# Performance work log

Hardware: AMD Instinct MI355X
Metric: run time of the kernel (lower is better)

Reference implementation:

```python
import jax, jax.numpy as jnp
import numpy as np

EMBED_DIM = 1024
NUM_HEADS = 16
HEAD_DIM = EMBED_DIM // NUM_HEADS


def setup_inputs() -> dict:
    key = jax.random.key(0)
    ks = jax.random.split(key, 7)
    B, S, E = 2, 2048, EMBED_DIM
    # xavier_uniform bound for square [E, E] weight
    bound = float(np.sqrt(6.0 / (E + E)))
    mkw = lambda k: jax.random.uniform(k, (E, E), jnp.float32, -bound, bound)
    return {
        "query": jax.random.normal(ks[0], (B, S, E), jnp.float32),
        "key": jax.random.normal(ks[1], (B, S, E), jnp.float32),
        "value": jax.random.normal(ks[2], (B, S, E), jnp.float32),
        "Wq": mkw(ks[3]),
        "Wk": mkw(ks[4]),
        "Wv": mkw(ks[5]),
        "Wo": mkw(ks[6]),
    }


def reference(query, key, value, Wq, Wk, Wv, Wo):
    # Chunked sigmoid attention: since sigmoid has no cross-key normalization
    # and all projections are bias-free linear maps, summing per-KV-chunk
    # partial outputs is mathematically identical to the full computation:
    #   out = (sigmoid(scale * Q K^T) @ V) @ Wo^T
    B, L, E = query.shape
    H, D = NUM_HEADS, HEAD_DIM
    scale = D ** -0.5
    q = (query @ Wq.T).reshape(B, L, H, D) * scale   # [B,L,H,D]
    k = (key @ Wk.T).reshape(B, -1, H, D)            # [B,S,H,D]
    v = (value @ Wv.T).reshape(B, -1, H, D)          # [B,S,H,D]
    scores = jax.nn.sigmoid(jnp.einsum('blhd,bshd->bhls', q, k))  # [B,H,L,S]
    o = jnp.einsum('bhls,bshd->blhd', scores, v).reshape(B, L, E)
    return o @ Wo.T
```

## Files before the change

### kernel.cpp

```cpp
#include <hip/hip_runtime.h>

typedef float f32x4 __attribute__((ext_vector_type(4)));
typedef float f32x16 __attribute__((ext_vector_type(16)));
typedef __bf16 bf16x4 __attribute__((ext_vector_type(4)));
typedef __bf16 bf16x8 __attribute__((ext_vector_type(8)));

constexpr int E = 1024;
constexpr int S = 2048;
constexpr int Bsz = 2;
constexpr int H = 16;
constexpr int Dh = 64;
constexpr int M = Bsz * S;

#define GLOAD_LDS16(g, l)                                                                 \
  __builtin_amdgcn_global_load_lds((const __attribute__((address_space(1))) void*)(g),    \
                                   (__attribute__((address_space(3))) void*)(l), 16, 0, 0)

__device__ __forceinline__ unsigned pk2(float a, float b) {
  union { __bf16 h[2]; unsigned u; } r;
  r.h[0] = (__bf16)a; r.h[1] = (__bf16)b;
  return r.u;
}

__global__ __launch_bounds__(256) void convert_bf16(
    const float* __restrict__ q, const float* __restrict__ k,
    const float* __restrict__ v, const float* __restrict__ wq,
    const float* __restrict__ wk, const float* __restrict__ wv,
    const float* __restrict__ wo, __bf16* __restrict__ aq,
    __bf16* __restrict__ ak, __bf16* __restrict__ av,
    __bf16* __restrict__ wqkv, __bf16* __restrict__ wob) {
  const int id = blockIdx.y;
  const float* src;
  __bf16* dst;
  int n;
  float scale = 1.0f;
  switch (id) {
    case 0: src = q;  dst = aq;             n = M * E; break;
    case 1: src = k;  dst = ak;             n = M * E; break;
    case 2: src = v;  dst = av;             n = M * E; break;
    case 3: src = wq; dst = wqkv;           n = E * E; scale = 0.125f; break;
    case 4: src = wk; dst = wqkv + E * E;   n = E * E; break;
    case 5: src = wv; dst = wqkv + 2 * E * E; n = E * E; break;
    default: src = wo; dst = wob;           n = E * E; break;
  }
  const int stride = gridDim.x * 256 * 8;
  for (int i = (blockIdx.x * 256 + threadIdx.x) * 8; i < n; i += stride) {
    f32x4 a = *reinterpret_cast<const f32x4*>(&src[i]);
    f32x4 b = *reinterpret_cast<const f32x4*>(&src[i + 4]);
    bf16x8 o;
    o[0] = (__bf16)(a[0] * scale); o[1] = (__bf16)(a[1] * scale);
    o[2] = (__bf16)(a[2] * scale); o[3] = (__bf16)(a[3] * scale);
    o[4] = (__bf16)(b[0] * scale); o[5] = (__bf16)(b[1] * scale);
    o[6] = (__bf16)(b[2] * scale); o[7] = (__bf16)(b[3] * scale);
    *reinterpret_cast<bf16x8*>(&dst[i]) = o;
  }
}

template <int TM, int MODE>
__global__ __launch_bounds__(256) void gemm_bf16nt(
    const __bf16* __restrict__ A0, const __bf16* __restrict__ A1,
    const __bf16* __restrict__ A2, const __bf16* __restrict__ Bw,
    void* __restrict__ C0, void* __restrict__ C1, void* __restrict__ C2) {
  constexpr int MI = TM / 32;
  __shared__ __bf16 As[TM][64];
  __shared__ __bf16 Bs[128][64];

  const int t    = threadIdx.x;
  const int lane = t & 63;
  const int wid  = t >> 6;
  const int wr   = (wid >> 1) * (TM / 2);
  const int wc   = (wid & 1) * 64;
  const int r16  = lane & 15;
  const int tm   = blockIdx.y * TM;
  const int tn   = blockIdx.x * 128;
  const int which = tn >> 10;

  const __bf16* Ab = (MODE == 0) ? (which == 0 ? A0 : which == 1 ? A1 : A2) : A0;

  f32x4 acc[MI][4] = {};

  for (int kt = 0; kt < E / 64; ++kt) {
    const int k0 = kt * 64;
    __syncthreads();
    constexpr int ACH = TM / 8;
    constexpr int NCH = ACH + 16;
#pragma unroll
    for (int c = wid; c < NCH; c += 4) {
      const bool isA = c < ACH;
      const int cc   = isA ? c : c - ACH;
      const int L    = cc * 1024 + lane * 16;
      const int row  = L >> 7;
      const int sw   = ((L >> 4) & 7) ^ (row & 7);
      const __bf16* src = isA ? &Ab[(size_t)(tm + row) * E + k0 + sw * 8]
                              : &Bw[(size_t)(tn + row) * E + k0 + sw * 8];
      char* dst = (isA ? (char*)As : (char*)Bs) + cc * 1024;
      GLOAD_LDS16(src, dst);
    }
    __syncthreads();
#pragma unroll
    for (int kc = 0; kc < 2; ++kc) {
      bf16x8 af[MI], bfv[4];
#pragma unroll
      for (int mi = 0; mi < MI; ++mi) {
        int row = wr + mi * 16 + r16;
        int g   = (kc * 4 + (lane >> 4)) ^ (row & 7);
        af[mi] = *reinterpret_cast<const bf16x8*>(&As[row][g * 8]);
      }
#pragma unroll
      for (int ni = 0; ni < 4; ++ni) {
        int row = wc + ni * 16 + r16;
        int g   = (kc * 4 + (lane >> 4)) ^ (row & 7);
        bfv[ni] = *reinterpret_cast<const bf16x8*>(&Bs[row][g * 8]);
      }
#pragma unroll
      for (int mi = 0; mi < MI; ++mi)
#pragma unroll
        for (int ni = 0; ni < 4; ++ni)
          acc[mi][ni] = __builtin_amdgcn_mfma_f32_16x16x32_bf16(af[mi], bfv[ni],
                                                                acc[mi][ni], 0, 0, 0);
    }
  }

#pragma unroll
  for (int mi = 0; mi < MI; ++mi) {
#pragma unroll
    for (int ni = 0; ni < 4; ++ni) {
#pragma unroll
      for (int j = 0; j < 4; ++j) {
        float v = acc[mi][ni][j];
        int m = tm + wr + mi * 16 + ((lane >> 4) << 2) + j;
        int n = tn + wc + ni * 16 + r16;
        if constexpr (MODE == 0) {
          int nl = n & 1023;
          int b = m >> 11, s = m & 2047, h = nl >> 6, d = nl & 63;
          __bf16* Cout = which == 0 ? (__bf16*)C0 : which == 1 ? (__bf16*)C1
                                                              : (__bf16*)C2;
          if (which < 2)
            Cout[((size_t)(b * H + h) * S + s) * Dh + d] = (__bf16)v;
          else
            Cout[((size_t)(b * H + h) * Dh + d) * S + s] = (__bf16)v;
        } else {
          ((float*)C0)[(size_t)m * E + n] = v;
        }
      }
    }
  }
}

__global__ __launch_bounds__(256) void attn_sigmoid(const __bf16* __restrict__ Q,
                                                    const __bf16* __restrict__ K,
                                                    const __bf16* __restrict__ Vt,
                                                    __bf16* __restrict__ O) {
  __shared__ char smem[128 * 72 * 2];
  __bf16* Ks = (__bf16*)smem;
  __bf16* Vs = (__bf16*)(smem + 8192);
  __bf16* Os = (__bf16*)smem;

  const int t    = threadIdx.x;
  const int lane = t & 63;
  const int wid  = t >> 6;
  const int l31  = lane & 31;
  const int hh   = lane >> 5;
  const int q0   = blockIdx.x * 128;
  const int h    = blockIdx.y;
  const int b    = blockIdx.z;

  const __bf16* Qh = Q + (size_t)(b * H + h) * S * Dh;
  const __bf16* Kh = K + (size_t)(b * H + h) * S * Dh;
  const __bf16* Vh = Vt + (size_t)(b * H + h) * Dh * S;

  bf16x8 Qf[4];
#pragma unroll
  for (int kc = 0; kc < 4; ++kc)
    Qf[kc] = *reinterpret_cast<const bf16x8*>(
        &Qh[(size_t)(q0 + wid * 32 + l31) * Dh + kc * 16 + hh * 8]);

  f32x16 ot[2] = {};

  for (int st = 0; st < S / 64; ++st) {
    __syncthreads();
#pragma unroll
    for (int j = 0; j < 2; ++j) {
      int base = (wid * 2 + j) * 1024;
      int L    = base + lane * 16;
      int row  = L >> 7;
      int x    = (L >> 4) & 7;
      int sw   = ((x ^ (row & 7)) * 8);
      GLOAD_LDS16(&Kh[(size_t)(st * 64 + row) * Dh + sw], (char*)Ks + base);
      GLOAD_LDS16(&Vh[(size_t)row * S + st * 64 + sw], (char*)Vs + base);
    }
    __syncthreads();

#pragma unroll
    for (int si = 0; si < 2; ++si) {
      f32x16 sacc = {};
#pragma unroll
      for (int kc = 0; kc < 4; ++kc) {
        int row = si * 32 + l31;
        int x = (2 * kc + hh) ^ (row & 7);
        bf16x8 kf = *reinterpret_cast<const bf16x8*>(&Ks[row * 64 + x * 8]);
        sacc = __builtin_amdgcn_mfma_f32_32x32x16_bf16(kf, Qf[kc], sacc, 0, 0, 0);
      }
      float p[16];
#pragma unroll
      for (int r = 0; r < 16; ++r)
        p[r] = __builtin_amdgcn_rcpf(1.0f + __expf(-sacc[r]));
      unsigned A0 = pk2(p[0], p[1]),   A1 = pk2(p[2], p[3]);
      unsigned B0 = pk2(p[4], p[5]),   B1 = pk2(p[6], p[7]);
      unsigned C0 = pk2(p[8], p[9]),   C1 = pk2(p[10], p[11]);
      unsigned D0 = pk2(p[12], p[13]), D1 = pk2(p[14], p[15]);
      unsigned W0 = __shfl_xor((int)(hh ? A0 : B0), 32, 64);
      unsigned W1 = __shfl_xor((int)(hh ? A1 : B1), 32, 64);
      unsigned W2 = __shfl_xor((int)(hh ? C0 : D0), 32, 64);
      unsigned W3 = __shfl_xor((int)(hh ? C1 : D1), 32, 64);
      union { unsigned u[4]; bf16x8 v; } f0, f1;
      f0.u[0] = hh ? W0 : A0;  f0.u[1] = hh ? W1 : A1;
      f0.u[2] = hh ? B0 : W0;  f0.u[3] = hh ? B1 : W1;
      f1.u[0] = hh ? W2 : C0;  f1.u[1] = hh ? W3 : C1;
      f1.u[2] = hh ? D0 : W2;  f1.u[3] = hh ? D1 : W3;

#pragma unroll
      for (int dblk = 0; dblk < 2; ++dblk) {
        int row = dblk * 32 + l31;
        int c0 = si * 2;
        int x0 = (2 * c0 + hh) ^ (row & 7);
        int x1 = (2 * (c0 + 1) + hh) ^ (row & 7);
        bf16x8 vf0 = *reinterpret_cast<const bf16x8*>(&Vs[row * 64 + x0 * 8]);
        bf16x8 vf1 = *reinterpret_cast<const bf16x8*>(&Vs[row * 64 + x1 * 8]);
        ot[dblk] = __builtin_amdgcn_mfma_f32_32x32x16_bf16(vf0, f0.v, ot[dblk], 0, 0, 0);
        ot[dblk] = __builtin_amdgcn_mfma_f32_32x32x16_bf16(vf1, f1.v, ot[dblk], 0, 0, 0);
      }
    }
  }

  __syncthreads();
#pragma unroll
  for (int dblk = 0; dblk < 2; ++dblk) {
#pragma unroll
    for (int rp = 0; rp < 8; ++rp) {
      int r = rp * 2;
      int d0 = dblk * 32 + (r & 3) + 8 * (r >> 2) + 4 * hh;
      unsigned u = pk2(ot[dblk][r], ot[dblk][r + 1]);
      *reinterpret_cast<unsigned*>(&Os[(wid * 32 + l31) * 72 + d0]) = u;
    }
  }
  __syncthreads();
#pragma unroll
  for (int i = 0; i < 4; ++i) {
    int c = i * 256 + t;
    int row = c >> 3;
    int ch = c & 7;
    bf16x8 v = *reinterpret_cast<const bf16x8*>(&Os[row * 72 + ch * 8]);
    *reinterpret_cast<bf16x8*>(&O[((size_t)(b * S) + q0 + row) * E + h * Dh + ch * 8]) = v;
  }
}

extern "C" void kernel_launch(void* const* d_in, const int* in_sizes, int n_in,
                              void* d_out, int out_size, void* d_ws, size_t ws_size,
                              hipStream_t stream) {
  const float* query = (const float*)d_in[0];
  const float* key_  = (const float*)d_in[1];
  const float* value = (const float*)d_in[2];
  const float* Wq    = (const float*)d_in[3];
  const float* Wk    = (const float*)d_in[4];
  const float* Wv    = (const float*)d_in[5];
  const float* Wo    = (const float*)d_in[6];

  char* ws = (char*)d_ws;
  __bf16* aq   = (__bf16*)(ws);
  __bf16* ak   = (__bf16*)(ws + ((size_t)8 << 20));
  __bf16* av   = (__bf16*)(ws + ((size_t)16 << 20));
  __bf16* wqkv = (__bf16*)(ws + ((size_t)24 << 20));
  __bf16* wob  = (__bf16*)(ws + ((size_t)30 << 20));
  __bf16* pq   = (__bf16*)(ws + ((size_t)32 << 20));
  __bf16* pk   = (__bf16*)(ws + ((size_t)40 << 20));
  __bf16* pvt  = (__bf16*)(ws + ((size_t)48 << 20));
  __bf16* ob   = (__bf16*)(ws);

  convert_bf16<<<dim3(512, 7), 256, 0, stream>>>(query, key_, value, Wq, Wk, Wv,
                                                 Wo, aq, ak, av, wqkv, wob);

  gemm_bf16nt<128, 0><<<dim3(3072 / 128, M / 128), 256, 0, stream>>>(
      aq, ak, av, wqkv, pq, pk, pvt);

  attn_sigmoid<<<dim3(S / 128, H, Bsz), 256, 0, stream>>>(pq, pk, pvt, ob);

  gemm_bf16nt<64, 2><<<dim3(E / 128, M / 64), 256, 0, stream>>>(
      ob, nullptr, nullptr, wob, (float*)d_out, nullptr, nullptr);
}
```

Before: 160.1 us.

## Double-buffer K/V tiles in sigmoid attention and fold log2e into Q scale

The attention kernel now uses 128-thread blocks over 64 query rows and double-buffers K/V tiles in LDS, issuing the next tile's async loads before computing the current one. This leaves one barrier per iteration. The Q weight scale now includes -log2(e), so sigmoid becomes rcp(1+exp2(x)) with no negate or multiply. The V-transpose store permutes sequence indices so the P fragments feed the PV MFMA directly without cross-lane shuffles. Output staging uses an XOR-swizzled LDS layout, and setprio hints are placed around the MFMA phases. The trade-off is more blocks, each holding 32KB of LDS, and a tighter coupling between the projection GEMM's store layout and the attention kernel.

```diff
diff --git a/kernel.cpp b/kernel.cpp
--- a/kernel.cpp
+++ b/kernel.cpp
@@ -38,7 +38,7 @@
     case 0: src = q;  dst = aq;             n = M * E; break;
     case 1: src = k;  dst = ak;             n = M * E; break;
     case 2: src = v;  dst = av;             n = M * E; break;
-    case 3: src = wq; dst = wqkv;           n = E * E; scale = 0.125f; break;
+    case 3: src = wq; dst = wqkv;           n = E * E; scale = -0.18033688f; break;
     case 4: src = wk; dst = wqkv + E * E;   n = E * E; break;
     case 5: src = wv; dst = wqkv + 2 * E * E; n = E * E; break;
     default: src = wo; dst = wob;           n = E * E; break;
@@ -135,10 +135,12 @@
           int b = m >> 11, s = m & 2047, h = nl >> 6, d = nl & 63;
           __bf16* Cout = which == 0 ? (__bf16*)C0 : which == 1 ? (__bf16*)C1
                                                               : (__bf16*)C2;
-          if (which < 2)
+          if (which < 2) {
             Cout[((size_t)(b * H + h) * S + s) * Dh + d] = (__bf16)v;
-          else
-            Cout[((size_t)(b * H + h) * Dh + d) * S + s] = (__bf16)v;
+          } else {
+            int ssw = (s & ~12) | ((s & 4) << 1) | ((s & 8) >> 1);
+            Cout[((size_t)(b * H + h) * Dh + d) * S + ssw] = (__bf16)v;
+          }
         } else {
           ((float*)C0)[(size_t)m * E + n] = v;
         }
@@ -147,21 +149,18 @@
   }
 }
 
-__global__ __launch_bounds__(256) void attn_sigmoid(const __bf16* __restrict__ Q,
+__global__ __launch_bounds__(128) void attn_sigmoid(const __bf16* __restrict__ Q,
                                                     const __bf16* __restrict__ K,
                                                     const __bf16* __restrict__ Vt,
                                                     __bf16* __restrict__ O) {
-  __shared__ char smem[128 * 72 * 2];
-  __bf16* Ks = (__bf16*)smem;
-  __bf16* Vs = (__bf16*)(smem + 8192);
-  __bf16* Os = (__bf16*)smem;
+  __shared__ char smem[2][16384];
 
   const int t    = threadIdx.x;
   const int lane = t & 63;
   const int wid  = t >> 6;
   const int l31  = lane & 31;
   const int hh   = lane >> 5;
-  const int q0   = blockIdx.x * 128;
+  const int q0   = blockIdx.x * 64;
   const int h    = blockIdx.y;
   const int b    = blockIdx.z;
 
@@ -169,88 +168,118 @@
   const __bf16* Kh = K + (size_t)(b * H + h) * S * Dh;
   const __bf16* Vh = Vt + (size_t)(b * H + h) * Dh * S;
 
+  auto stage = [&](int st, int pb) {
+    char* bK = &smem[pb][0];
+    char* bV = &smem[pb][8192];
+#pragma unroll
+    for (int j = 0; j < 4; ++j) {
+      int base = (wid * 4 + j) * 1024;
+      int L    = base + lane * 16;
+      int row  = L >> 7;
+      int sw   = ((L >> 4) & 7) ^ (row & 7);
+      GLOAD_LDS16(&Kh[(size_t)(st * 64 + row) * Dh + sw * 8], bK + base);
+      GLOAD_LDS16(&Vh[(size_t)row * S + st * 64 + sw * 8], bV + base);
+    }
+  };
+
+  stage(0, 0);
+
   bf16x8 Qf[4];
 #pragma unroll
   for (int kc = 0; kc < 4; ++kc)
     Qf[kc] = *reinterpret_cast<const bf16x8*>(
         &Qh[(size_t)(q0 + wid * 32 + l31) * Dh + kc * 16 + hh * 8]);
 
-  f32x16 ot[2] = {};
+  f32x16 ot0 = {}, ot1 = {};
+  __syncthreads();
 
   for (int st = 0; st < S / 64; ++st) {
-    __syncthreads();
-#pragma unroll
-    for (int j = 0; j < 2; ++j) {
-      int base = (wid * 2 + j) * 1024;
-      int L    = base + lane * 16;
-      int row  = L >> 7;
-      int x    = (L >> 4) & 7;
-      int sw   = ((x ^ (row & 7)) * 8);
-      GLOAD_LDS16(&Kh[(size_t)(st * 64 + row) * Dh + sw], (char*)Ks + base);
-      GLOAD_LDS16(&Vh[(size_t)row * S + st * 64 + sw], (char*)Vs + base);
-    }
-    __syncthreads();
-
-#pragma unroll
-    for (int si = 0; si < 2; ++si) {
-      f32x16 sacc = {};
-#pragma unroll
-      for (int kc = 0; kc < 4; ++kc) {
-        int row = si * 32 + l31;
-        int x = (2 * kc + hh) ^ (row & 7);
-        bf16x8 kf = *reinterpret_cast<const bf16x8*>(&Ks[row * 64 + x * 8]);
-        sacc = __builtin_amdgcn_mfma_f32_32x32x16_bf16(kf, Qf[kc], sacc, 0, 0, 0);
-      }
-      float p[16];
-#pragma unroll
-      for (int r = 0; r < 16; ++r)
-        p[r] = __builtin_amdgcn_rcpf(1.0f + __expf(-sacc[r]));
-      unsigned A0 = pk2(p[0], p[1]),   A1 = pk2(p[2], p[3]);
-      unsigned B0 = pk2(p[4], p[5]),   B1 = pk2(p[6], p[7]);
-      unsigned C0 = pk2(p[8], p[9]),   C1 = pk2(p[10], p[11]);
-      unsigned D0 = pk2(p[12], p[13]), D1 = pk2(p[14], p[15]);
-      unsigned W0 = __shfl_xor((int)(hh ? A0 : B0), 32, 64);
-      unsigned W1 = __shfl_xor((int)(hh ? A1 : B1), 32, 64);
-      unsigned W2 = __shfl_xor((int)(hh ? C0 : D0), 32, 64);
-      unsigned W3 = __shfl_xor((int)(hh ? C1 : D1), 32, 64);
-      union { unsigned u[4]; bf16x8 v; } f0, f1;
-      f0.u[0] = hh ? W0 : A0;  f0.u[1] = hh ? W1 : A1;
-      f0.u[2] = hh ? B0 : W0;  f0.u[3] = hh ? B1 : W1;
-      f1.u[0] = hh ? W2 : C0;  f1.u[1] = hh ? W3 : C1;
-      f1.u[2] = hh ? D0 : W2;  f1.u[3] = hh ? D1 : W3;
-
+    const int cur = st & 1;
+    if (st + 1 < S / 64) stage(st + 1, cur ^ 1);
+
+    const __bf16* Ks = (const __bf16*)&smem[cur][0];
+    const __bf16* Vs = (const __bf16*)(&smem[cur][8192]);
+
+    f32x16 s0 = {}, s1 = {};
+    __builtin_amdgcn_s_setprio(1);
+#pragma unroll
+    for (int kc = 0; kc < 4; ++kc) {
+      int x = (2 * kc + hh) ^ (l31 & 7);
+      bf16x8 k0 = *reinterpret_cast<const bf16x8*>(&Ks[l31 * 64 + x * 8]);
+      bf16x8 k1 = *reinterpret_cast<const bf16x8*>(&Ks[(32 + l31) * 64 + x * 8]);
+      s0 = __builtin_amdgcn_mfma_f32_32x32x16_bf16(k0, Qf[kc], s0, 0, 0, 0);
+      s1 = __builtin_amdgcn_mfma_f32_32x32x16_bf16(k1, Qf[kc], s1, 0, 0, 0);
+    }
+    __builtin_amdgcn_s_setprio(0);
+
+    bf16x8 vf[8];
+#pragma unroll
+    for (int c = 0; c < 4; ++c) {
 #pragma unroll
       for (int dblk = 0; dblk < 2; ++dblk) {
         int row = dblk * 32 + l31;
-        int c0 = si * 2;
-        int x0 = (2 * c0 + hh) ^ (row & 7);
-        int x1 = (2 * (c0 + 1) + hh) ^ (row & 7);
-        bf16x8 vf0 = *reinterpret_cast<const bf16x8*>(&Vs[row * 64 + x0 * 8]);
-        bf16x8 vf1 = *reinterpret_cast<const bf16x8*>(&Vs[row * 64 + x1 * 8]);
-        ot[dblk] = __builtin_amdgcn_mfma_f32_32x32x16_bf16(vf0, f0.v, ot[dblk], 0, 0, 0);
-        ot[dblk] = __builtin_amdgcn_mfma_f32_32x32x16_bf16(vf1, f1.v, ot[dblk], 0, 0, 0);
-      }
-    }
-  }
-
+        int x   = (2 * c + hh) ^ (row & 7);
+        vf[c * 2 + dblk] = *reinterpret_cast<const bf16x8*>(&Vs[row * 64 + x * 8]);
+      }
+    }
+
+    bf16x8 F[4];
+    {
+      union { unsigned u[4]; bf16x8 v; } fu[4];
+#pragma unroll
+      for (int c = 0; c < 4; ++c) {
+        int base = (c & 1) * 8;
+#pragma unroll
+        for (int jj = 0; jj < 4; ++jj) {
+          float ya = (c < 2) ? s0[base + 2 * jj] : s1[base + 2 * jj];
+          float yb = (c < 2) ? s0[base + 2 * jj + 1] : s1[base + 2 * jj + 1];
+          float pa = __builtin_amdgcn_rcpf(1.0f + __builtin_amdgcn_exp2f(ya));
+          float pb = __builtin_amdgcn_rcpf(1.0f + __builtin_amdgcn_exp2f(yb));
+          fu[c].u[jj] = pk2(pa, pb);
+        }
+        F[c] = fu[c].v;
+      }
+    }
+
+    __builtin_amdgcn_s_setprio(1);
+#pragma unroll
+    for (int c = 0; c < 4; ++c) {
+      ot0 = __builtin_amdgcn_mfma_f32_32x32x16_bf16(vf[c * 2 + 0], F[c], ot0, 0, 0, 0);
+      ot1 = __builtin_amdgcn_mfma_f32_32x32x16_bf16(vf[c * 2 + 1], F[c], ot1, 0, 0, 0);
+    }
+    __builtin_amdgcn_s_setprio(0);
+
+    __syncthreads();
+  }
+
+  __bf16* Os = (__bf16*)&smem[0][0];
+  {
+    int row = wid * 32 + l31;
+#pragma unroll
+    for (int dblk = 0; dblk < 2; ++dblk) {
+#pragma unroll
+      for (int rp = 0; rp < 4; ++rp) {
+        int r  = rp * 4;
+        int g  = dblk * 4 + rp;
+        int by = row * 128 + ((g ^ (row & 7)) * 16) + hh * 8;
+        float a0 = dblk ? ot1[r]     : ot0[r];
+        float a1 = dblk ? ot1[r + 1] : ot0[r + 1];
+        float a2 = dblk ? ot1[r + 2] : ot0[r + 2];
+        float a3 = dblk ? ot1[r + 3] : ot0[r + 3];
+        unsigned long long val =
+            (unsigned long long)pk2(a0, a1) | ((unsigned long long)pk2(a2, a3) << 32);
+        *reinterpret_cast<unsigned long long*>((char*)Os + by) = val;
+      }
+    }
+  }
   __syncthreads();
 #pragma unroll
-  for (int dblk = 0; dblk < 2; ++dblk) {
-#pragma unroll
-    for (int rp = 0; rp < 8; ++rp) {
-      int r = rp * 2;
-      int d0 = dblk * 32 + (r & 3) + 8 * (r >> 2) + 4 * hh;
-      unsigned u = pk2(ot[dblk][r], ot[dblk][r + 1]);
-      *reinterpret_cast<unsigned*>(&Os[(wid * 32 + l31) * 72 + d0]) = u;
-    }
-  }
-  __syncthreads();
-#pragma unroll
   for (int i = 0; i < 4; ++i) {
-    int c = i * 256 + t;
+    int c   = i * 128 + t;
     int row = c >> 3;
-    int ch = c & 7;
-    bf16x8 v = *reinterpret_cast<const bf16x8*>(&Os[row * 72 + ch * 8]);
+    int ch  = c & 7;
+    bf16x8 v = *reinterpret_cast<const bf16x8*>(
+        (char*)Os + row * 128 + ((ch ^ (row & 7)) * 16));
     *reinterpret_cast<bf16x8*>(&O[((size_t)(b * S) + q0 + row) * E + h * Dh + ch * 8]) = v;
   }
 }
@@ -283,7 +312,7 @@
   gemm_bf16nt<128, 0><<<dim3(3072 / 128, M / 128), 256, 0, stream>>>(
       aq, ak, av, wqkv, pq, pk, pvt);
 
-  attn_sigmoid<<<dim3(S / 128, H, Bsz), 256, 0, stream>>>(pq, pk, pvt, ob);
+  attn_sigmoid<<<dim3(S / 64, H, Bsz), 128, 0, stream>>>(pq, pk, pvt, ob);
 
   gemm_bf16nt<64, 2><<<dim3(E / 128, M / 64), 256, 0, stream>>>(
       ob, nullptr, nullptr, wob, (float*)d_out, nullptr, nullptr);
```

Result: faster. 154.3 us (-3.7%).
